# Performance work log

Measured on AMD Instinct MI355X. Metric: run time of the kernel, lower is better.

## Reference

```python
import jax, jax.numpy as jnp
import numpy as np

D = 1024      # mapped_dim
M = 5         # num_ref_modes
H = 112
W = 112


def setup_inputs() -> dict:
    key = jax.random.key(0)
    ks = jax.random.split(key, 9)
    roi_signal = jax.random.randint(ks[0], (1, 1, H, W), 0, M, dtype=jnp.int32)
    roi_features = jax.random.normal(ks[1], (1, D, H, W), dtype=jnp.float32)
    roi_mask = jax.random.uniform(ks[2], (1, 1, H, W), dtype=jnp.float32)
    s = np.float32(1.0 / np.sqrt(D))
    patch_embed = jax.random.normal(ks[3], (M, D), dtype=jnp.float32) * np.float32(np.sqrt(2.0 / (M + D)))
    Wq = jax.random.normal(ks[4], (D, D), dtype=jnp.float32) * s
    Wk = jax.random.normal(ks[5], (D, D), dtype=jnp.float32) * s
    Wv = jax.random.normal(ks[6], (D, D), dtype=jnp.float32) * s
    bq = jnp.zeros((D,), jnp.float32)
    bk = jnp.zeros((D,), jnp.float32)
    bv = jnp.zeros((D,), jnp.float32)
    conv_w = jax.random.normal(ks[7], (1, D), dtype=jnp.float32) * s  # 1x1 conv, out=1
    conv_b = jnp.zeros((1,), jnp.float32)
    return dict(roi_signal=roi_signal, roi_features=roi_features, roi_mask=roi_mask,
                patch_embed=patch_embed, Wq=Wq, bq=bq, Wk=Wk, bk=bk, Wv=Wv, bv=bv,
                conv_w=conv_w, conv_b=conv_b)


def reference(roi_signal, roi_features, roi_mask, patch_embed, Wq, bq, Wk, bk, Wv, bv, conv_w, conv_b):
    _, _, ROI_H, ROI_W = roi_mask.shape
    d = roi_features.shape[1]
    # ref_embed: one_hot(ref_label) @ patch_embed == gather; (1,1,H,W) -> (1,H,W,D) -> (1,D,H,W)
    pe = jnp.transpose(patch_embed[roi_signal[:, 0]], (0, 3, 1, 2))
    xA = roi_features + pe
    # flatten to tokens: (D, N).T -> (N, D)
    A = xA.reshape(d, -1).T
    O = roi_features.reshape(d, -1).T
    Q = A @ Wq.T + bq
    K = O @ Wk.T + bk
    V = O @ Wv.T + bv
    scores = (Q @ K.T) / jnp.sqrt(jnp.float32(d))        # (N, N) -- dominant intermediate
    attn = jax.nn.softmax(scores, axis=-1)
    out = attn @ V                                        # (N, D)
    # 1x1 conv classification head == per-token dot with conv_w
    seg = (out @ conv_w.T + conv_b).reshape(1, 1, ROI_H, ROI_W)
    return jax.nn.sigmoid(seg.astype(jnp.float32))
```

## Files before the change

kernel.cpp:

```cpp
#include <hip/hip_runtime.h>
#include <math.h>


#define DD 1024
#define NN 12544
#define NSPLIT 5
#define NPART  10
#define NTILES 49

typedef __attribute__((ext_vector_type(8))) short short8;
typedef __attribute__((ext_vector_type(4))) float f32x4;
typedef __attribute__((ext_vector_type(4))) unsigned short ushort4_t;
typedef unsigned short ushort_t;
typedef unsigned int uint32;

__device__ __forceinline__ ushort_t f2bf(float f) {
    union { float f; uint32 u; } v; v.f = f;
    uint32 u = v.u + 0x7FFF + ((v.u >> 16) & 1);
    return (ushort_t)(u >> 16);
}

__device__ __forceinline__ void gload_lds16(const void* g, void* l) {
    __builtin_amdgcn_global_load_lds((const __attribute__((address_space(1))) uint32*)g,
                                     (__attribute__((address_space(3))) uint32*)l, 16, 0, 0);
}

__global__ void k_u(const float* __restrict__ Wv, const float* __restrict__ cw,
                    const float* __restrict__ bv, float* __restrict__ u,
                    float* __restrict__ cptr) {
    const int t = threadIdx.x;
    const int k = blockIdx.x * 256 + t;
    const int d0 = blockIdx.y * 64;
    float acc = 0.f;
#pragma unroll 16
    for (int i = 0; i < 64; ++i) acc += Wv[(size_t)(d0 + i) * DD + k] * cw[d0 + i];
    atomicAdd(&u[k], acc);
    if (blockIdx.x == 0 && t < 64) {
        float ca = bv[d0 + t] * cw[d0 + t];
        for (int off = 32; off > 0; off >>= 1) ca += __shfl_down(ca, off);
        if (t == 0) atomicAdd(cptr, ca);
    }
}

__global__ __launch_bounds__(256)
void k_prep(const float* __restrict__ rf, const int* __restrict__ sig,
            const float* __restrict__ pe, const float* __restrict__ u,
            ushort_t* __restrict__ xo, ushort_t* __restrict__ xa,
            float* __restrict__ vsc) {
    __shared__ ushort_t so[64][136];
    __shared__ ushort_t sa[64][136];
    __shared__ float pel[5 * 128];
    __shared__ float ul[128];
    __shared__ int sigl[64];
    __shared__ f32x4 red[16][16];
    const int t = threadIdx.x;
    const int n0 = blockIdx.x * 64;
    if (t < 64) sigl[t] = sig[n0 + t];
    __syncthreads();
    const int dl = t >> 4, tg = t & 15;
    const int sg[4] = {sigl[tg * 4], sigl[tg * 4 + 1], sigl[tg * 4 + 2], sigl[tg * 4 + 3]};
    const int tok = t >> 2, part = t & 3;
    f32x4 vacc = (f32x4)(0.f);

    for (int c = 0; c < 8; ++c) {
        const int d0 = c * 128;
        for (int i = t; i < 640; i += 256) pel[i] = pe[(i >> 7) * DD + d0 + (i & 127)];
        if (t < 128) ul[t] = u[d0 + t];
        __syncthreads();
#pragma unroll
        for (int s = 0; s < 8; ++s) {
            const int dli = s * 16 + dl;
            const f32x4 x = *(const f32x4*)&rf[(size_t)(d0 + dli) * NN + n0 + tg * 4];
            vacc += x * ul[dli];
            ushort_t oo[4], aa[4];
#pragma unroll
            for (int j = 0; j < 4; ++j) {
                oo[j] = f2bf(x[j]);
                aa[j] = f2bf(x[j] + pel[sg[j] * 128 + dli]);
            }
#pragma unroll
            for (int j = 0; j < 4; ++j) {
                so[tg * 4 + j][dli] = oo[j];
                sa[tg * 4 + j][dli] = aa[j];
            }
        }
        __syncthreads();
#pragma unroll
        for (int i = 0; i < 4; ++i) {
            const int off = part * 32 + i * 8;
            *(short8*)&xo[(size_t)(n0 + tok) * DD + d0 + off] = *(const short8*)&so[tok][off];
            *(short8*)&xa[(size_t)(n0 + tok) * DD + d0 + off] = *(const short8*)&sa[tok][off];
        }
        __syncthreads();
    }
    red[dl][tg] = vacc;
    __syncthreads();
    if (t < 64) {
        float s = 0.f;
#pragma unroll
        for (int i = 0; i < 16; ++i) s += ((const float*)&red[i][t >> 2])[t & 3];
        vsc[n0 + t] = s;
    }
}

__global__ void k_wcast(const float* __restrict__ Wq, const float* __restrict__ Wk,
                        ushort_t* __restrict__ wqb, ushort_t* __restrict__ wkb) {
    const int idx = (blockIdx.x * 256 + threadIdx.x) * 8;
    const float* src = blockIdx.y ? Wk : Wq;
    ushort_t* dst = blockIdx.y ? wkb : wqb;
    f32x4 a = *(const f32x4*)&src[idx];
    f32x4 b = *(const f32x4*)&src[idx + 4];
    short8 o;
#pragma unroll
    for (int j = 0; j < 4; ++j) { o[j] = (short)f2bf(a[j]); o[4 + j] = (short)f2bf(b[j]); }
    *(short8*)&dst[idx] = o;
}

__global__ __launch_bounds__(256, 2)
void k_pgemm(const ushort_t* __restrict__ xb, const ushort_t* __restrict__ wb,
             const float* __restrict__ bias, float scale, ushort_t* __restrict__ outb) {
    __shared__ ushort_t as_[128 * 64];
    __shared__ ushort_t bs_[128 * 64];
    const int t = threadIdx.x;
    const int wv = t >> 6, ln = t & 63;
    const int wr = wv >> 1, wc = wv & 1;
    const int l15 = ln & 15, lhi = ln >> 4;
    const int n0 = blockIdx.x * 128;
    const int m0 = blockIdx.y * 128;
    const int srow = wv * 32;
    const int lr = ln >> 3, lc = ln & 7;
    const int swz = lc ^ lr;

    f32x4 acc[4][4];
#pragma unroll
    for (int a = 0; a < 4; ++a)
#pragma unroll
        for (int b = 0; b < 4; ++b) acc[a][b] = (f32x4)(0.f);

    for (int kk = 0; kk < DD; kk += 64) {
        __syncthreads();
#pragma unroll
        for (int i = 0; i < 4; ++i) {
            const int tok = srow + i * 8 + lr;
            gload_lds16(wb + (size_t)(m0 + tok) * DD + kk + (swz << 3), as_ + (srow + i * 8) * 64);
            gload_lds16(xb + (size_t)(n0 + tok) * DD + kk + (swz << 3), bs_ + (srow + i * 8) * 64);
        }
        __syncthreads();
#pragma unroll
        for (int kp = 0; kp < 2; ++kp) {
            short8 af[4], bf_[4];
#pragma unroll
            for (int mi = 0; mi < 4; ++mi) {
                int r = wr * 64 + mi * 16 + l15;
                int cch = (kp * 4 + lhi) ^ (r & 7);
                af[mi] = *(const short8*)(as_ + r * 64 + cch * 8);
            }
#pragma unroll
            for (int ni = 0; ni < 4; ++ni) {
                int r = wc * 64 + ni * 16 + l15;
                int cch = (kp * 4 + lhi) ^ (r & 7);
                bf_[ni] = *(const short8*)(bs_ + r * 64 + cch * 8);
            }
#pragma unroll
            for (int mi = 0; mi < 4; ++mi)
#pragma unroll
                for (int ni = 0; ni < 4; ++ni)
                    acc[mi][ni] = __builtin_amdgcn_mfma_f32_16x16x32_bf16(
                        af[mi], bf_[ni], acc[mi][ni], 0, 0, 0);
        }
    }
    float bb[4][4];
#pragma unroll
    for (int mi = 0; mi < 4; ++mi) {
        f32x4 b4 = *(const f32x4*)&bias[m0 + wr * 64 + mi * 16 + lhi * 4];
#pragma unroll
        for (int r = 0; r < 4; ++r) bb[mi][r] = b4[r];
    }
#pragma unroll
    for (int mi = 0; mi < 4; ++mi)
#pragma unroll
        for (int ni = 0; ni < 4; ++ni) {
            ushort4_t o;
#pragma unroll
            for (int r = 0; r < 4; ++r) o[r] = f2bf((acc[mi][ni][r] + bb[mi][r]) * scale);
            *(ushort4_t*)&outb[(size_t)(n0 + wc * 64 + ni * 16 + l15) * DD +
                               m0 + wr * 64 + mi * 16 + lhi * 4] = o;
        }
}

__global__ __launch_bounds__(512, 2)
void k_attn(const ushort_t* __restrict__ qb, const ushort_t* __restrict__ kb,
            const float* __restrict__ vsc, float* __restrict__ pm,
            float* __restrict__ pl, float* __restrict__ pa) {
    __shared__ ushort_t As[2][256 * 64];
    __shared__ ushort_t Bs[2][256 * 64];
    const int t = threadIdx.x;
    const int wv = t >> 6, ln = t & 63;
    const int wm = wv >> 1, wn = wv & 1;
    const int l15 = ln & 15, lhi = ln >> 4;

    const int g = blockIdx.x;
    const int xcd = g & 7, gq = g >> 3;
    const int L = (xcd < 5) ? xcd * 31 + gq : 155 + (xcd - 5) * 30 + gq;
    const int bx = L / NSPLIT, split = L % NSPLIT;
    const int m0 = bx * 256;

    const int srw = (ln >> 3);
    const int sch = ln & 7;

    float rm[4][4], rl[4][4], ra[4][4];
#pragma unroll
    for (int a = 0; a < 4; ++a)
#pragma unroll
        for (int b = 0; b < 4; ++b) { rm[a][b] = -INFINITY; rl[a][b] = 0.f; ra[a][b] = 0.f; }

    f32x4 acc[4][8];
#pragma unroll
    for (int a = 0; a < 4; ++a)
#pragma unroll
        for (int b = 0; b < 8; ++b) acc[a][b] = (f32x4)(0.f);

    int cur = 0;
    {
        const int n0 = split * 256;
#pragma unroll
        for (int b = 0; b < 4; ++b) {
            const int r = b * 64 + wv * 8 + srw;
            const int soff = (sch ^ (r & 7)) << 3;
            gload_lds16(qb + (size_t)(m0 + r) * DD + soff, &As[0][(b * 64 + wv * 8) * 64]);
            gload_lds16(kb + (size_t)(n0 + r) * DD + soff, &Bs[0][(b * 64 + wv * 8) * 64]);
        }
    }
    asm volatile("s_waitcnt vmcnt(0)" ::: "memory");
    __builtin_amdgcn_s_barrier();

    for (int nt = split; nt < NTILES; nt += NSPLIT) {
        const int n0 = nt * 256;
        for (int kidx = 0; kidx < 16; ++kidx) {
            int nk = kidx + 1, nnt = nt;
            if (nk == 16) { nk = 0; nnt = nt + NSPLIT; }
            if (nnt < NTILES) {
                const int kko = nk * 64;
                const int nn0 = nnt * 256;
                ushort_t* Ad = &As[cur ^ 1][0];
                ushort_t* Bd = &Bs[cur ^ 1][0];
#pragma unroll
                for (int b = 0; b < 4; ++b) {
                    const int r = b * 64 + wv * 8 + srw;
                    const int soff = kko + ((sch ^ (r & 7)) << 3);
                    gload_lds16(qb + (size_t)(m0 + r) * DD + soff, Ad + (b * 64 + wv * 8) * 64);
                    gload_lds16(kb + (size_t)(nn0 + r) * DD + soff, Bd + (b * 64 + wv * 8) * 64);
                }
            }
            const ushort_t* Ab = &As[cur][0];
            const ushort_t* Bb = &Bs[cur][0];
#pragma unroll
            for (int kp = 0; kp < 2; ++kp) {
                short8 af[4], bfr[8];
#pragma unroll
                for (int mi = 0; mi < 4; ++mi) {
                    const int r = wm * 64 + mi * 16 + l15;
                    const int c = (kp * 4 + lhi) ^ (r & 7);
                    af[mi] = *(const short8*)(Ab + r * 64 + c * 8);
                }
#pragma unroll
                for (int ni = 0; ni < 8; ++ni) {
                    const int r = wn * 128 + ni * 16 + l15;
                    const int c = (kp * 4 + lhi) ^ (r & 7);
                    bfr[ni] = *(const short8*)(Bb + r * 64 + c * 8);
                }
                __builtin_amdgcn_s_setprio(1);
#pragma unroll
                for (int ni = 0; ni < 8; ++ni)
#pragma unroll
                    for (int mi = 0; mi < 4; ++mi)
                        acc[mi][ni] = __builtin_amdgcn_mfma_f32_16x16x32_bf16(
                            af[mi], bfr[ni], acc[mi][ni], 0, 0, 0);
                __builtin_amdgcn_s_setprio(0);
            }
            if (kidx == 15) {
                float vv[8];
#pragma unroll
                for (int ni = 0; ni < 8; ++ni) vv[ni] = vsc[n0 + wn * 128 + ni * 16 + l15];
#pragma unroll
                for (int mi = 0; mi < 4; ++mi) {
#pragma unroll
                    for (int r = 0; r < 4; ++r) {
                        float mx = acc[mi][0][r];
#pragma unroll
                        for (int ni = 1; ni < 8; ++ni) mx = fmaxf(mx, acc[mi][ni][r]);
                        mx = fmaxf(mx, __shfl_xor(mx, 1));
                        mx = fmaxf(mx, __shfl_xor(mx, 2));
                        mx = fmaxf(mx, __shfl_xor(mx, 4));
                        mx = fmaxf(mx, __shfl_xor(mx, 8));
                        const float mnew = fmaxf(rm[mi][r], mx);
                        float sp = 0.f, sv = 0.f;
#pragma unroll
                        for (int ni = 0; ni < 8; ++ni) {
                            float p = __expf(acc[mi][ni][r] - mnew);
                            sp += p; sv += p * vv[ni];
                        }
                        sp += __shfl_xor(sp, 1); sv += __shfl_xor(sv, 1);
                        sp += __shfl_xor(sp, 2); sv += __shfl_xor(sv, 2);
                        sp += __shfl_xor(sp, 4); sv += __shfl_xor(sv, 4);
                        sp += __shfl_xor(sp, 8); sv += __shfl_xor(sv, 8);
                        const float f = __expf(rm[mi][r] - mnew);
                        rl[mi][r] = rl[mi][r] * f + sp;
                        ra[mi][r] = ra[mi][r] * f + sv;
                        rm[mi][r] = mnew;
                    }
                }
#pragma unroll
                for (int a = 0; a < 4; ++a)
#pragma unroll
                    for (int b = 0; b < 8; ++b) acc[a][b] = (f32x4)(0.f);
            }
            asm volatile("s_waitcnt vmcnt(0)" ::: "memory");
            __builtin_amdgcn_s_barrier();
            cur ^= 1;
        }
    }
    if (l15 == 0) {
        const size_t slab = (size_t)(split * 2 + wn) * NN;
#pragma unroll
        for (int mi = 0; mi < 4; ++mi)
#pragma unroll
            for (int r = 0; r < 4; ++r) {
                int row = m0 + wm * 64 + mi * 16 + lhi * 4 + r;
                pm[slab + row] = rm[mi][r];
                pl[slab + row] = rl[mi][r];
                pa[slab + row] = ra[mi][r];
            }
    }
}

__global__ void k_comb(const float* __restrict__ pm, const float* __restrict__ pl,
                       const float* __restrict__ pa, const float* __restrict__ cptr,
                       const float* __restrict__ cb, float* __restrict__ out) {
    int n = blockIdx.x * 256 + threadIdx.x;
    float gm = -INFINITY;
#pragma unroll
    for (int s = 0; s < NPART; ++s) gm = fmaxf(gm, pm[(size_t)s * NN + n]);
    float l = 0.f, a = 0.f;
#pragma unroll
    for (int s = 0; s < NPART; ++s) {
        float f = __expf(pm[(size_t)s * NN + n] - gm);
        l += pl[(size_t)s * NN + n] * f;
        a += pa[(size_t)s * NN + n] * f;
    }
    float x = a / l + cptr[0] + cb[0];
    out[n] = 1.f / (1.f + __expf(-x));
}

extern "C" void kernel_launch(void* const* d_in, const int* in_sizes, int n_in,
                              void* d_out, int out_size, void* d_ws, size_t ws_size,
                              hipStream_t stream) {
    const int* sig = (const int*)d_in[0];
    const float* rf = (const float*)d_in[1];
    const float* pe = (const float*)d_in[3];
    const float* Wq = (const float*)d_in[4];
    const float* bq = (const float*)d_in[5];
    const float* Wk = (const float*)d_in[6];
    const float* bk = (const float*)d_in[7];
    const float* Wv = (const float*)d_in[8];
    const float* bv = (const float*)d_in[9];
    const float* cw = (const float*)d_in[10];
    const float* cb = (const float*)d_in[11];
    float* out = (float*)d_out;

    ushort_t* buf0 = (ushort_t*)d_ws;
    ushort_t* buf1 = buf0 + (size_t)NN * DD;
    ushort_t* buf2 = buf1 + (size_t)NN * DD;
    ushort_t* wqb = buf2 + (size_t)NN * DD;
    ushort_t* wkb = wqb + (size_t)DD * DD;
    float* u = (float*)(wkb + (size_t)DD * DD);
    float* cptr = u + 1024;
    float* vsc = u + 1024 + 16;
    float* pm = vsc + NN;
    float* pl = pm + (size_t)NPART * NN;
    float* pa = pl + (size_t)NPART * NN;

    hipMemsetAsync(u, 0, (1024 + 16) * sizeof(float), stream);
    k_u<<<dim3(4, 16), 256, 0, stream>>>(Wv, cw, bv, u, cptr);
    k_prep<<<196, 256, 0, stream>>>(rf, sig, pe, u, buf0, buf1, vsc);
    k_wcast<<<dim3(512, 2), 256, 0, stream>>>(Wq, Wk, wqb, wkb);
    k_pgemm<<<dim3(98, 8), 256, 0, stream>>>(buf0, wkb, bk, 1.0f, buf2);
    k_pgemm<<<dim3(98, 8), 256, 0, stream>>>(buf1, wqb, bq, 0.03125f, buf0);
    k_attn<<<245, 512, 0, stream>>>(buf0, buf2, vsc, pm, pl, pa);
    k_comb<<<NN / 256, 256, 0, stream>>>(pm, pl, pa, cptr, cb, out);
}
```

Measured before the change: 484.3 us.

## Interleave global-to-LDS staging with MFMA phases in QK attention loop

Splits each k-step into four phases, each issuing one slice of the next tile's global-to-LDS loads, reading a half of the B fragments and running 16 MFMAs, with barriers and sched_barrier between phases. The aim is to spread memory traffic across the compute instead of issuing it all up front, and to shrink the live B-fragment registers from 8 to 4. In exchange it adds several extra workgroup barriers per k-step, which can add synchronisation stalls.

```diff
diff --git a/kernel.cpp b/kernel.cpp
--- a/kernel.cpp
+++ b/kernel.cpp
@@ -234,50 +234,65 @@
     asm volatile("s_waitcnt vmcnt(0)" ::: "memory");
     __builtin_amdgcn_s_barrier();
 
+#define PHASE(P, KP, NH, READA)                                                   \
+    {                                                                             \
+        if (do_stage) {                                                           \
+            const int rr = (P) * 64 + wv * 8 + srw;                               \
+            const int soff = kko + ((sch ^ (rr & 7)) << 3);                       \
+            gload_lds16(qb + (size_t)(m0 + rr) * DD + soff,                       \
+                        Ad + ((P) * 64 + wv * 8) * 64);                           \
+            gload_lds16(kb + (size_t)(nn0 + rr) * DD + soff,                      \
+                        Bd + ((P) * 64 + wv * 8) * 64);                           \
+        }                                                                         \
+        if (READA) {                                                              \
+            _Pragma("unroll")                                                     \
+            for (int mi = 0; mi < 4; ++mi) {                                      \
+                const int r = wm * 64 + mi * 16 + l15;                            \
+                const int c = ((KP) * 4 + lhi) ^ (r & 7);                         \
+                af[mi] = *(const short8*)(Ab + r * 64 + c * 8);                   \
+            }                                                                     \
+        }                                                                         \
+        _Pragma("unroll")                                                         \
+        for (int ni = 0; ni < 4; ++ni) {                                          \
+            const int r = wn * 128 + (NH) * 64 + ni * 16 + l15;                   \
+            const int c = ((KP) * 4 + lhi) ^ (r & 7);                             \
+            bfr[ni] = *(const short8*)(Bb + r * 64 + c * 8);                      \
+        }                                                                         \
+        __builtin_amdgcn_s_barrier();                                             \
+        asm volatile("s_waitcnt lgkmcnt(0)" ::: "memory");                        \
+        __builtin_amdgcn_sched_barrier(0);                                        \
+        __builtin_amdgcn_s_setprio(1);                                            \
+        _Pragma("unroll")                                                         \
+        for (int ni = 0; ni < 4; ++ni)                                            \
+            _Pragma("unroll")                                                     \
+            for (int mi = 0; mi < 4; ++mi)                                        \
+                acc[mi][(NH) * 4 + ni] = __builtin_amdgcn_mfma_f32_16x16x32_bf16( \
+                    af[mi], bfr[ni], acc[mi][(NH) * 4 + ni], 0, 0, 0);            \
+        __builtin_amdgcn_s_setprio(0);                                            \
+    }
+
     for (int nt = split; nt < NTILES; nt += NSPLIT) {
         const int n0 = nt * 256;
         for (int kidx = 0; kidx < 16; ++kidx) {
             int nk = kidx + 1, nnt = nt;
             if (nk == 16) { nk = 0; nnt = nt + NSPLIT; }
-            if (nnt < NTILES) {
-                const int kko = nk * 64;
-                const int nn0 = nnt * 256;
-                ushort_t* Ad = &As[cur ^ 1][0];
-                ushort_t* Bd = &Bs[cur ^ 1][0];
-#pragma unroll
-                for (int b = 0; b < 4; ++b) {
-                    const int r = b * 64 + wv * 8 + srw;
-                    const int soff = kko + ((sch ^ (r & 7)) << 3);
-                    gload_lds16(qb + (size_t)(m0 + r) * DD + soff, Ad + (b * 64 + wv * 8) * 64);
-                    gload_lds16(kb + (size_t)(nn0 + r) * DD + soff, Bd + (b * 64 + wv * 8) * 64);
-                }
-            }
+            const bool do_stage = (nnt < NTILES);
+            const int kko = nk * 64;
+            const int nn0 = nnt * 256;
+            ushort_t* Ad = &As[cur ^ 1][0];
+            ushort_t* Bd = &Bs[cur ^ 1][0];
             const ushort_t* Ab = &As[cur][0];
             const ushort_t* Bb = &Bs[cur][0];
-#pragma unroll
-            for (int kp = 0; kp < 2; ++kp) {
-                short8 af[4], bfr[8];
-#pragma unroll
-                for (int mi = 0; mi < 4; ++mi) {
-                    const int r = wm * 64 + mi * 16 + l15;
-                    const int c = (kp * 4 + lhi) ^ (r & 7);
-                    af[mi] = *(const short8*)(Ab + r * 64 + c * 8);
-                }
-#pragma unroll
-                for (int ni = 0; ni < 8; ++ni) {
-                    const int r = wn * 128 + ni * 16 + l15;
-                    const int c = (kp * 4 + lhi) ^ (r & 7);
-                    bfr[ni] = *(const short8*)(Bb + r * 64 + c * 8);
-                }
-                __builtin_amdgcn_s_setprio(1);
-#pragma unroll
-                for (int ni = 0; ni < 8; ++ni)
-#pragma unroll
-                    for (int mi = 0; mi < 4; ++mi)
-                        acc[mi][ni] = __builtin_amdgcn_mfma_f32_16x16x32_bf16(
-                            af[mi], bfr[ni], acc[mi][ni], 0, 0, 0);
-                __builtin_amdgcn_s_setprio(0);
-            }
+            short8 af[4], bfr[4];
+
+            PHASE(0, 0, 0, true);
+            __builtin_amdgcn_s_barrier();
+            PHASE(1, 0, 1, false);
+            __builtin_amdgcn_s_barrier();
+            PHASE(2, 1, 0, true);
+            __builtin_amdgcn_s_barrier();
+            PHASE(3, 1, 1, false);
+
             if (kidx == 15) {
                 float vv[8];
 #pragma unroll
@@ -320,6 +335,7 @@
             cur ^= 1;
         }
     }
+#undef PHASE
     if (l15 == 0) {
         const size_t slab = (size_t)(split * 2 + wn) * NN;
 #pragma unroll
```

New measurement: 644.3 us. 1.33x slower.

## Shrink attention tile to 128x256 with K-step 32 and 256-thread blocks

Applied to the files above, without the earlier changes.

Reshapes the attention score kernel from 256x256 tiles with a 64-wide K step and 512 threads into 128x256 tiles with a 32-wide K step and 256 threads. The grid doubles to 490 blocks, the XCD mapping is rewritten for 2 remaining tiles per XCD, and the LDS swizzle is adapted to 32-column rows. The aim is a smaller LDS footprint and better occupancy and load balance across CUs. In exchange, each Q tile is reused less, K is loaded twice as often, and there are twice as many barriers per tile.

```diff
diff --git a/kernel.cpp b/kernel.cpp
--- a/kernel.cpp
+++ b/kernel.cpp
@@ -188,12 +188,12 @@
         }
 }
 
-__global__ __launch_bounds__(512, 2)
+__global__ __launch_bounds__(256, 2)
 void k_attn(const ushort_t* __restrict__ qb, const ushort_t* __restrict__ kb,
             const float* __restrict__ vsc, float* __restrict__ pm,
             float* __restrict__ pl, float* __restrict__ pa) {
-    __shared__ ushort_t As[2][256 * 64];
-    __shared__ ushort_t Bs[2][256 * 64];
+    __shared__ ushort_t As[2][128 * 32];
+    __shared__ ushort_t Bs[2][256 * 32];
     const int t = threadIdx.x;
     const int wv = t >> 6, ln = t & 63;
     const int wm = wv >> 1, wn = wv & 1;
@@ -201,12 +201,12 @@
 
     const int g = blockIdx.x;
     const int xcd = g & 7, gq = g >> 3;
-    const int L = (xcd < 5) ? xcd * 31 + gq : 155 + (xcd - 5) * 30 + gq;
+    const int L = (xcd < 2) ? xcd * 62 + gq : 124 + (xcd - 2) * 61 + gq;
     const int bx = L / NSPLIT, split = L % NSPLIT;
-    const int m0 = bx * 256;
-
-    const int srw = (ln >> 3);
-    const int sch = ln & 7;
+    const int m0 = bx * 128;
+
+    const int srr = ln >> 2;
+    const int slc = ln & 3;
 
     float rm[4][4], rl[4][4], ra[4][4];
 #pragma unroll
@@ -224,11 +224,16 @@
     {
         const int n0 = split * 256;
 #pragma unroll
-        for (int b = 0; b < 4; ++b) {
-            const int r = b * 64 + wv * 8 + srw;
-            const int soff = (sch ^ (r & 7)) << 3;
-            gload_lds16(qb + (size_t)(m0 + r) * DD + soff, &As[0][(b * 64 + wv * 8) * 64]);
-            gload_lds16(kb + (size_t)(n0 + r) * DD + soff, &Bs[0][(b * 64 + wv * 8) * 64]);
+        for (int i = 0; i < 2; ++i) {
+            const int row = wv * 32 + i * 16 + srr;
+            const int sc = slc ^ ((row >> 1) & 3);
+            gload_lds16(qb + (size_t)(m0 + row) * DD + sc * 8, &As[0][(wv * 32 + i * 16) * 32]);
+        }
+#pragma unroll
+        for (int i = 0; i < 4; ++i) {
+            const int row = wv * 64 + i * 16 + srr;
+            const int sc = slc ^ ((row >> 1) & 3);
+            gload_lds16(kb + (size_t)(n0 + row) * DD + sc * 8, &Bs[0][(wv * 64 + i * 16) * 32]);
         }
     }
     asm volatile("s_waitcnt vmcnt(0)" ::: "memory");
@@ -236,49 +241,54 @@
 
     for (int nt = split; nt < NTILES; nt += NSPLIT) {
         const int n0 = nt * 256;
-        for (int kidx = 0; kidx < 16; ++kidx) {
+        for (int kidx = 0; kidx < 32; ++kidx) {
             int nk = kidx + 1, nnt = nt;
-            if (nk == 16) { nk = 0; nnt = nt + NSPLIT; }
+            if (nk == 32) { nk = 0; nnt = nt + NSPLIT; }
             if (nnt < NTILES) {
-                const int kko = nk * 64;
+                const int kko = nk * 32;
                 const int nn0 = nnt * 256;
                 ushort_t* Ad = &As[cur ^ 1][0];
                 ushort_t* Bd = &Bs[cur ^ 1][0];
 #pragma unroll
-                for (int b = 0; b < 4; ++b) {
-                    const int r = b * 64 + wv * 8 + srw;
-                    const int soff = kko + ((sch ^ (r & 7)) << 3);
-                    gload_lds16(qb + (size_t)(m0 + r) * DD + soff, Ad + (b * 64 + wv * 8) * 64);
-                    gload_lds16(kb + (size_t)(nn0 + r) * DD + soff, Bd + (b * 64 + wv * 8) * 64);
+                for (int i = 0; i < 2; ++i) {
+                    const int row = wv * 32 + i * 16 + srr;
+                    const int sc = slc ^ ((row >> 1) & 3);
+                    gload_lds16(qb + (size_t)(m0 + row) * DD + kko + sc * 8,
+                                Ad + (wv * 32 + i * 16) * 32);
+                }
+#pragma unroll
+                for (int i = 0; i < 4; ++i) {
+                    const int row = wv * 64 + i * 16 + srr;
+                    const int sc = slc ^ ((row >> 1) & 3);
+                    gload_lds16(kb + (size_t)(nn0 + row) * DD + kko + sc * 8,
+                                Bd + (wv * 64 + i * 16) * 32);
                 }
             }
             const ushort_t* Ab = &As[cur][0];
             const ushort_t* Bb = &Bs[cur][0];
-#pragma unroll
-            for (int kp = 0; kp < 2; ++kp) {
-                short8 af[4], bfr[8];
-#pragma unroll
-                for (int mi = 0; mi < 4; ++mi) {
-                    const int r = wm * 64 + mi * 16 + l15;
-                    const int c = (kp * 4 + lhi) ^ (r & 7);
-                    af[mi] = *(const short8*)(Ab + r * 64 + c * 8);
-                }
-#pragma unroll
-                for (int ni = 0; ni < 8; ++ni) {
-                    const int r = wn * 128 + ni * 16 + l15;
-                    const int c = (kp * 4 + lhi) ^ (r & 7);
-                    bfr[ni] = *(const short8*)(Bb + r * 64 + c * 8);
-                }
-                __builtin_amdgcn_s_setprio(1);
-#pragma unroll
-                for (int ni = 0; ni < 8; ++ni)
-#pragma unroll
-                    for (int mi = 0; mi < 4; ++mi)
-                        acc[mi][ni] = __builtin_amdgcn_mfma_f32_16x16x32_bf16(
-                            af[mi], bfr[ni], acc[mi][ni], 0, 0, 0);
-                __builtin_amdgcn_s_setprio(0);
-            }
-            if (kidx == 15) {
+            short8 af[4], bfr[8];
+#pragma unroll
+            for (int mi = 0; mi < 4; ++mi) {
+                const int r = wm * 64 + mi * 16 + l15;
+                const int c = lhi ^ ((r >> 1) & 3);
+                af[mi] = *(const short8*)(Ab + r * 32 + c * 8);
+            }
+#pragma unroll
+            for (int ni = 0; ni < 8; ++ni) {
+                const int r = wn * 128 + ni * 16 + l15;
+                const int c = lhi ^ ((r >> 1) & 3);
+                bfr[ni] = *(const short8*)(Bb + r * 32 + c * 8);
+            }
+            __builtin_amdgcn_s_setprio(1);
+#pragma unroll
+            for (int ni = 0; ni < 8; ++ni)
+#pragma unroll
+                for (int mi = 0; mi < 4; ++mi)
+                    acc[mi][ni] = __builtin_amdgcn_mfma_f32_16x16x32_bf16(
+                        af[mi], bfr[ni], acc[mi][ni], 0, 0, 0);
+            __builtin_amdgcn_s_setprio(0);
+
+            if (kidx == 31) {
                 float vv[8];
 #pragma unroll
                 for (int ni = 0; ni < 8; ++ni) vv[ni] = vsc[n0 + wn * 128 + ni * 16 + l15];
@@ -386,6 +396,6 @@
     k_wcast<<<dim3(512, 2), 256, 0, stream>>>(Wq, Wk, wqb, wkb);
     k_pgemm<<<dim3(98, 8), 256, 0, stream>>>(buf0, wkb, bk, 1.0f, buf2);
     k_pgemm<<<dim3(98, 8), 256, 0, stream>>>(buf1, wqb, bq, 0.03125f, buf0);
-    k_attn<<<245, 512, 0, stream>>>(buf0, buf2, vsc, pm, pl, pa);
+    k_attn<<<490, 256, 0, stream>>>(buf0, buf2, vsc, pm, pl, pa);
     k_comb<<<NN / 256, 256, 0, stream>>>(pm, pl, pa, cptr, cb, out);
 }
```

Measured after the change: 496.6 us. 1.03x slower.
